# Optimization experiments

Measured on AMD Instinct MI355X. Metric: run time of the kernel, lower is better.

## Reference

```python
import jax, jax.numpy as jnp
import numpy as np

N_NODES = 100000
N_EDGES = 3200000
IN_DIM = 512
OUT_DIM = 256


def setup_inputs() -> dict:
    key = jax.random.key(0)
    k1, k2, k3, k4, k5 = jax.random.split(key, 5)
    features = jax.random.normal(k1, (N_NODES, IN_DIM), dtype=jnp.float32)
    adj_rows = jax.random.randint(k2, (N_EDGES,), 0, N_NODES, dtype=jnp.int32)
    adj_cols = jax.random.randint(k3, (N_EDGES,), 0, N_NODES, dtype=jnp.int32)
    # normalized adjacency values (e.g., 1/sqrt(d_i d_j)); random positive here
    adj_vals = jax.random.uniform(k4, (N_EDGES,), dtype=jnp.float32) * (1.0 / 32.0)
    # xavier uniform for kernel
    limit = np.sqrt(6.0 / (IN_DIM + OUT_DIM)).astype(np.float32)
    kernel = jax.random.uniform(k5, (IN_DIM, OUT_DIM), dtype=jnp.float32, minval=-limit, maxval=limit)
    bias = jnp.zeros((OUT_DIM,), dtype=jnp.float32)
    skip_weight = jnp.ones((OUT_DIM,), dtype=jnp.float32)
    return {
        "features": features,
        "adj_rows": adj_rows,
        "adj_cols": adj_cols,
        "adj_vals": adj_vals,
        "kernel": kernel,
        "bias": bias,
        "skip_weight": skip_weight,
    }


def reference(features, adj_rows, adj_cols, adj_vals, kernel, bias, skip_weight):
    # dense feature transform: [N, in] @ [in, out] -> [N, out]
    xw = jnp.matmul(features, kernel)
    # SpMM: aggregate[i] = sum_e val[e] * xw[col[e]] over edges with row[e] == i
    msgs = adj_vals[:, None] * xw[adj_cols]            # [E, out] gather
    agg = jax.ops.segment_sum(msgs, adj_rows, num_segments=N_NODES)  # [N, out] scatter-add
    out = xw * skip_weight + agg + bias                # skip scale + bias epilogue
    return jax.nn.selu(out)
```

## Files before the change

### kernel.cpp

```cpp
#include <hip/hip_runtime.h>
#include <hip/hip_bf16.h>
#include <cstdint>
#include <cstddef>

#define IN_DIM 512
#define OUT_DIM 256
#define BROWS 256
#define NBUCK_MAX 512

typedef __bf16 bf16x8 __attribute__((ext_vector_type(8)));
typedef float f32x4 __attribute__((ext_vector_type(4)));

__device__ __forceinline__ unsigned short f2bf(float f) {
    __bf16 h = (__bf16)f;
    return __builtin_bit_cast(unsigned short, h);
}
__device__ __forceinline__ float bf2f(unsigned short u) {
    unsigned int x = ((unsigned int)u) << 16;
    return __builtin_bit_cast(float, x);
}
__device__ __forceinline__ float selu(float x) {
    const float kScale = 1.0507009873554805f;
    const float kAlpha = 1.6732632423543772f;
    return (x > 0.f) ? kScale * x : kScale * kAlpha * (expf(x) - 1.f);
}

__global__ void k_convW(const float* __restrict__ W, unsigned short* __restrict__ Wt) {
    int idx = blockIdx.x * 256 + threadIdx.x;
    int n = idx & (OUT_DIM - 1);
    int k = idx >> 8;
    if (k < IN_DIM) Wt[n * IN_DIM + k] = f2bf(W[k * OUT_DIM + n]);
}

__launch_bounds__(512, 2)
__global__ void k_gemm(const float* __restrict__ A, const unsigned short* __restrict__ Wt,
                       signed char* __restrict__ xq, float* __restrict__ scales, int M) {
    __shared__ unsigned short lA[128 * 32];
    __shared__ unsigned short lB[256 * 32];
    __shared__ float lrm[128];
    const int t = threadIdx.x;
    const int wave = t >> 6, lane = t & 63;
    const int wr = wave >> 2, wc = wave & 3;
    const int m0 = blockIdx.x * 128;
    const int mlo = lane & 15, kq = lane >> 4;

    if (t < 128) lrm[t] = 0.f;

    f32x4 acc[4][4] = {};

    for (int k0 = 0; k0 < IN_DIM; k0 += 32) {
        #pragma unroll
        for (int p = 0; p < 2; ++p) {
            int idx = p * 512 + t;
            int r = idx >> 3, c4 = idx & 7;
            int gr = m0 + r; if (gr >= M) gr = M - 1;
            const float4 v = *reinterpret_cast<const float4*>(&A[(size_t)gr * IN_DIM + k0 + c4 * 4]);
            ushort4 u;
            u.x = f2bf(v.x); u.y = f2bf(v.y); u.z = f2bf(v.z); u.w = f2bf(v.w);
            *reinterpret_cast<ushort4*>(&lA[r * 32 + c4 * 4]) = u;
        }
        #pragma unroll
        for (int p = 0; p < 2; ++p) {
            int idx = p * 512 + t;
            int n = idx >> 2, c8 = idx & 3;
            const uint4 v = *reinterpret_cast<const uint4*>(&Wt[(size_t)n * IN_DIM + k0 + c8 * 8]);
            *reinterpret_cast<uint4*>(&lB[n * 32 + c8 * 8]) = v;
        }
        __syncthreads();

        bf16x8 af[4], bfr[4];
        #pragma unroll
        for (int mt = 0; mt < 4; ++mt)
            af[mt] = *reinterpret_cast<const bf16x8*>(&lA[(wr * 64 + mt * 16 + mlo) * 32 + kq * 8]);
        #pragma unroll
        for (int nt = 0; nt < 4; ++nt)
            bfr[nt] = *reinterpret_cast<const bf16x8*>(&lB[(wc * 64 + nt * 16 + mlo) * 32 + kq * 8]);
        #pragma unroll
        for (int mt = 0; mt < 4; ++mt)
            #pragma unroll
            for (int nt = 0; nt < 4; ++nt)
                acc[mt][nt] = __builtin_amdgcn_mfma_f32_16x16x32_bf16(af[mt], bfr[nt], acc[mt][nt], 0, 0, 0);
        __syncthreads();
    }

    #pragma unroll
    for (int mt = 0; mt < 4; ++mt) {
        #pragma unroll
        for (int i = 0; i < 4; ++i) {
            float m = fmaxf(fmaxf(fabsf(acc[mt][0][i]), fabsf(acc[mt][1][i])),
                            fmaxf(fabsf(acc[mt][2][i]), fabsf(acc[mt][3][i])));
            m = fmaxf(m, __shfl_xor(m, 1));
            m = fmaxf(m, __shfl_xor(m, 2));
            m = fmaxf(m, __shfl_xor(m, 4));
            m = fmaxf(m, __shfl_xor(m, 8));
            if (mlo == 0)
                atomicMax(reinterpret_cast<int*>(&lrm[wr * 64 + mt * 16 + kq * 4 + i]),
                          __float_as_int(m));
        }
    }
    __syncthreads();

    #pragma unroll
    for (int mt = 0; mt < 4; ++mt) {
        #pragma unroll
        for (int i = 0; i < 4; ++i) {
            const int rl = wr * 64 + mt * 16 + kq * 4 + i;
            const int row = m0 + rl;
            const float rm = lrm[rl];
            const float inv = (rm > 0.f) ? (127.f / rm) : 0.f;
            if (row < M) {
                #pragma unroll
                for (int nt = 0; nt < 4; ++nt) {
                    int q = (int)rintf(acc[mt][nt][i] * inv);
                    xq[(size_t)row * OUT_DIM + wc * 64 + nt * 16 + mlo] = (signed char)q;
                }
            }
        }
    }
    if (t < 128) {
        int row = m0 + t;
        if (row < M) scales[row] = lrm[t] * (1.f / 127.f);
    }
}

__launch_bounds__(512)
__global__ void k_bhist(const int* __restrict__ rows, int* __restrict__ bcnt, int E) {
    __shared__ int cnt[NBUCK_MAX];
    const int t = threadIdx.x;
    const int base = blockIdx.x * 8192;
    cnt[t] = 0;
    __syncthreads();
    #pragma unroll
    for (int p = 0; p < 4; ++p) {
        const int i = base + p * 2048 + (t << 2);
        if (i + 4 <= E) {
            int4 r4 = *reinterpret_cast<const int4*>(&rows[i]);
            atomicAdd(&cnt[r4.x >> 8], 1);
            atomicAdd(&cnt[r4.y >> 8], 1);
            atomicAdd(&cnt[r4.z >> 8], 1);
            atomicAdd(&cnt[r4.w >> 8], 1);
        } else if (i < E) {
            for (int j = i; j < E && j < i + 4; ++j) atomicAdd(&cnt[rows[j] >> 8], 1);
        }
    }
    __syncthreads();
    if (cnt[t] > 0) atomicAdd(&bcnt[t], cnt[t]);
}

__launch_bounds__(NBUCK_MAX)
__global__ void k_bscan(const int* __restrict__ bcnt, int* __restrict__ bbase,
                        int* __restrict__ bcursor, int nbuck, int E) {
    const int t = threadIdx.x;
    __shared__ int sh[NBUCK_MAX];
    int v = (t < nbuck) ? bcnt[t] : 0;
    sh[t] = v;
    __syncthreads();
    for (int off = 1; off < NBUCK_MAX; off <<= 1) {
        int x = (t >= off) ? sh[t - off] : 0;
        __syncthreads();
        sh[t] += x;
        __syncthreads();
    }
    int ex = sh[t] - v;
    bbase[t] = ex;
    bcursor[t] = ex;
    if (t == 0) bbase[NBUCK_MAX] = E;
}

__launch_bounds__(512)
__global__ void k_bin(const int* __restrict__ rows, const int* __restrict__ cols,
                      const float* __restrict__ vals, int* __restrict__ bcursor,
                      int2* __restrict__ binned, int E) {
    __shared__ int cnt[NBUCK_MAX];
    __shared__ int scn[NBUCK_MAX];
    __shared__ int dlt[NBUCK_MAX];
    const int t = threadIdx.x;
    const int base = blockIdx.x * 8192;

    cnt[t] = 0;
    __syncthreads();

    int er[16], ec[16];
    float ev[16];
    #pragma unroll
    for (int p = 0; p < 4; ++p) {
        const int i = base + p * 2048 + (t << 2);
        if (i + 4 <= E) {
            int4 r4 = *reinterpret_cast<const int4*>(&rows[i]);
            int4 c4 = *reinterpret_cast<const int4*>(&cols[i]);
            float4 v4 = *reinterpret_cast<const float4*>(&vals[i]);
            er[4*p+0] = r4.x; ec[4*p+0] = c4.x; ev[4*p+0] = v4.x;
            er[4*p+1] = r4.y; ec[4*p+1] = c4.y; ev[4*p+1] = v4.y;
            er[4*p+2] = r4.z; ec[4*p+2] = c4.z; ev[4*p+2] = v4.z;
            er[4*p+3] = r4.w; ec[4*p+3] = c4.w; ev[4*p+3] = v4.w;
        } else {
            #pragma unroll
            for (int j = 0; j < 4; ++j) {
                int idx = i + j;
                bool ok = idx < E;
                er[4*p+j] = ok ? rows[idx] : -1;
                ec[4*p+j] = ok ? cols[idx] : 0;
                ev[4*p+j] = ok ? vals[idx] : 0.f;
            }
        }
    }

    #pragma unroll
    for (int k = 0; k < 16; ++k)
        if (er[k] >= 0) atomicAdd(&cnt[er[k] >> 8], 1);
    __syncthreads();

    int v = cnt[t];
    scn[t] = v;
    __syncthreads();
    for (int off = 1; off < NBUCK_MAX; off <<= 1) {
        int x = (t >= off) ? scn[t - off] : 0;
        __syncthreads();
        scn[t] += x;
        __syncthreads();
    }
    int ex = scn[t] - v;

    int d = 0;
    if (v > 0) d = atomicAdd(&bcursor[t], v) - ex;
    dlt[t] = d;
    cnt[t] = ex;
    __syncthreads();

    #pragma unroll
    for (int k = 0; k < 16; ++k) {
        if (er[k] >= 0) {
            int b = er[k] >> 8;
            int lp = atomicAdd(&cnt[b], 1);
            binned[(size_t)(dlt[b] + lp)] =
                make_int2(ec[k] | ((er[k] & 255) << 17), __float_as_int(ev[k]));
        }
    }
}

__launch_bounds__(256)
__global__ void k_fine2(const int2* __restrict__ binned, const int* __restrict__ bbase,
                        const float* __restrict__ scales, int2* __restrict__ ecv,
                        int* __restrict__ rs, int M, int E, int nbuck) {
    __shared__ int lcnt[BROWS];
    __shared__ int lcur[BROWS];
    const int b = blockIdx.x, t = threadIdx.x;
    const int r0 = b * BROWS;
    lcnt[t] = 0;
    const int start = __builtin_amdgcn_readfirstlane(bbase[b]);
    const int end   = __builtin_amdgcn_readfirstlane(bbase[b + 1]);
    __syncthreads();

    for (int i = start + t; i < end; i += 256)
        atomicAdd(&lcnt[binned[i].x >> 17], 1);
    __syncthreads();

    int v = lcnt[t];
    lcur[t] = v;
    __syncthreads();
    for (int off = 1; off < 256; off <<= 1) {
        int x = (t >= off) ? lcur[t - off] : 0;
        __syncthreads();
        lcur[t] += x;
        __syncthreads();
    }
    int rowoff = start + (lcur[t] - v);
    if (r0 + t < M) rs[r0 + t] = rowoff;
    if (b == nbuck - 1 && t == 0) rs[M] = E;
    lcur[t] = rowoff;
    __syncthreads();

    for (int i = start + t; i < end; i += 256) {
        int2 rec = binned[i];
        int r = rec.x >> 17;
        int col = rec.x & 0x1FFFF;
        int pos = atomicAdd(&lcur[r], 1);
        ecv[pos] = make_int2(col, __float_as_int(__int_as_float(rec.y) * scales[col]));
    }
}

__global__ void k_hist(const int* __restrict__ rows, int* __restrict__ counts, int E) {
    int i = (blockIdx.x * 256 + threadIdx.x) * 4;
    if (i + 4 <= E) {
        int4 r = *reinterpret_cast<const int4*>(&rows[i]);
        atomicAdd(&counts[r.x], 1);
        atomicAdd(&counts[r.y], 1);
        atomicAdd(&counts[r.z], 1);
        atomicAdd(&counts[r.w], 1);
    } else {
        for (int j = i; j < E; ++j) atomicAdd(&counts[rows[j]], 1);
    }
}

__global__ void k_scan1(const int* __restrict__ counts, int* __restrict__ rs,
                        int* __restrict__ bsum, int N) {
    int b = blockIdx.x, t = threadIdx.x;
    int base = b * 1024 + t * 4;
    int4 v = make_int4(0, 0, 0, 0);
    if (base + 4 <= N) v = *reinterpret_cast<const int4*>(&counts[base]);
    else {
        if (base + 0 < N) v.x = counts[base + 0];
        if (base + 1 < N) v.y = counts[base + 1];
        if (base + 2 < N) v.z = counts[base + 2];
        if (base + 3 < N) v.w = counts[base + 3];
    }
    int s0 = v.x, s1 = s0 + v.y, s2 = s1 + v.z, s3 = s2 + v.w;
    __shared__ int sh[256];
    sh[t] = s3; __syncthreads();
    for (int off = 1; off < 256; off <<= 1) {
        int x = (t >= off) ? sh[t - off] : 0;
        __syncthreads();
        sh[t] += x;
        __syncthreads();
    }
    int ex = sh[t] - s3;
    if (base + 0 < N) rs[base + 0] = ex;
    if (base + 1 < N) rs[base + 1] = ex + s0;
    if (base + 2 < N) rs[base + 2] = ex + s1;
    if (base + 3 < N) rs[base + 3] = ex + s2;
    if (t == 255) bsum[b] = sh[255];
}

__global__ void k_scan2(const int* __restrict__ bsum, int* __restrict__ boff, int nb) {
    int t = threadIdx.x;
    __shared__ int sh[256];
    int v = (t < nb) ? bsum[t] : 0;
    sh[t] = v; __syncthreads();
    for (int off = 1; off < 256; off <<= 1) {
        int x = (t >= off) ? sh[t - off] : 0;
        __syncthreads();
        sh[t] += x;
        __syncthreads();
    }
    if (t < nb) boff[t] = sh[t] - v;
}

__global__ void k_scan3(int* __restrict__ rs, int* __restrict__ cursor,
                        const int* __restrict__ boff, int N, int E) {
    int b = blockIdx.x, t = threadIdx.x;
    int base = b * 1024 + t * 4;
    int o = boff[b];
    #pragma unroll
    for (int j = 0; j < 4; ++j) {
        if (base + j < N) {
            int v = rs[base + j] + o;
            rs[base + j] = v;
            cursor[base + j] = v;
        }
    }
    if (b == 0 && t == 0) rs[N] = E;
}

__global__ void k_scatter(const int* __restrict__ rows, const int* __restrict__ cols,
                          const float* __restrict__ vals, const float* __restrict__ scales,
                          int* __restrict__ cursor, int2* __restrict__ ecv, int E) {
    int i = (blockIdx.x * 256 + threadIdx.x) * 4;
    if (i + 4 <= E) {
        int4 r = *reinterpret_cast<const int4*>(&rows[i]);
        int4 c = *reinterpret_cast<const int4*>(&cols[i]);
        float4 v = *reinterpret_cast<const float4*>(&vals[i]);
        int p0 = atomicAdd(&cursor[r.x], 1); ecv[p0] = make_int2(c.x, __float_as_int(v.x * scales[c.x]));
        int p1 = atomicAdd(&cursor[r.y], 1); ecv[p1] = make_int2(c.y, __float_as_int(v.y * scales[c.y]));
        int p2 = atomicAdd(&cursor[r.z], 1); ecv[p2] = make_int2(c.z, __float_as_int(v.z * scales[c.z]));
        int p3 = atomicAdd(&cursor[r.w], 1); ecv[p3] = make_int2(c.w, __float_as_int(v.w * scales[c.w]));
    } else {
        for (int j = i; j < E; ++j) {
            int p = atomicAdd(&cursor[rows[j]], 1);
            ecv[p] = make_int2(cols[j], __float_as_int(vals[j] * scales[cols[j]]));
        }
    }
}

__launch_bounds__(256)
__global__ void k_agg(const signed char* __restrict__ xq,
                      const float* __restrict__ scales,
                      const int2* __restrict__ ecv,
                      const int* __restrict__ rs,
                      const float* __restrict__ skipw,
                      const float* __restrict__ bias,
                      float* __restrict__ out, int M) {
    const int wave = threadIdx.x >> 6, lane = threadIdx.x & 63;
    const int node = blockIdx.x * 4 + wave;
    if (node >= M) return;
    const int s = __builtin_amdgcn_readfirstlane(rs[node]);
    const int e = __builtin_amdgcn_readfirstlane(rs[node + 1]);
    const int d4 = lane * 4;

    float a0 = 0.f, a1 = 0.f, a2 = 0.f, a3 = 0.f;
    int p = s;
    constexpr int U = 8;
    for (; p + U <= e; p += U) {
        int   cs[U];
        float vs[U];
        #pragma unroll
        for (int u = 0; u < U; ++u) {
            int2 c = ecv[p + u];
            cs[u] = c.x; vs[u] = __int_as_float(c.y);
        }
        int g[U];
        #pragma unroll
        for (int u = 0; u < U; ++u)
            g[u] = *reinterpret_cast<const int*>(&xq[(size_t)cs[u] * OUT_DIM + d4]);
        #pragma unroll
        for (int u = 0; u < U; ++u) {
            a0 += vs[u] * (float)(signed char)(g[u]);
            a1 += vs[u] * (float)(signed char)(g[u] >> 8);
            a2 += vs[u] * (float)(signed char)(g[u] >> 16);
            a3 += vs[u] * (float)(g[u] >> 24);
        }
    }
    for (; p < e; ++p) {
        int2 c = ecv[p];
        float v = __int_as_float(c.y);
        int g = *reinterpret_cast<const int*>(&xq[(size_t)c.x * OUT_DIM + d4]);
        a0 += v * (float)(signed char)(g);
        a1 += v * (float)(signed char)(g >> 8);
        a2 += v * (float)(signed char)(g >> 16);
        a3 += v * (float)(g >> 24);
    }

    int w = *reinterpret_cast<const int*>(&xq[(size_t)node * OUT_DIM + d4]);
    float sc = scales[node];
    float x0 = (float)(signed char)(w)        * sc;
    float x1 = (float)(signed char)(w >> 8)   * sc;
    float x2 = (float)(signed char)(w >> 16)  * sc;
    float x3 = (float)(w >> 24)               * sc;

    float4 sw = *reinterpret_cast<const float4*>(&skipw[d4]);
    float4 bi = *reinterpret_cast<const float4*>(&bias[d4]);
    float4 r;
    r.x = selu(a0 + x0 * sw.x + bi.x);
    r.y = selu(a1 + x1 * sw.y + bi.y);
    r.z = selu(a2 + x2 * sw.z + bi.z);
    r.w = selu(a3 + x3 * sw.w + bi.w);
    *reinterpret_cast<float4*>(&out[(size_t)node * OUT_DIM + d4]) = r;
}

extern "C" void kernel_launch(void* const* d_in, const int* in_sizes, int n_in,
                              void* d_out, int out_size, void* d_ws, size_t ws_size,
                              hipStream_t stream) {
    const float* features = (const float*)d_in[0];
    const int*   adj_rows = (const int*)d_in[1];
    const int*   adj_cols = (const int*)d_in[2];
    const float* adj_vals = (const float*)d_in[3];
    const float* Wk       = (const float*)d_in[4];
    const float* bias     = (const float*)d_in[5];
    const float* skipw    = (const float*)d_in[6];
    float* out = (float*)d_out;

    const int M = in_sizes[0] / IN_DIM;
    const int E = in_sizes[1];

    char* w = (char*)d_ws;
    size_t off = 0;
    auto carve = [&](size_t bytes) -> void* {
        void* p = w + off;
        off = (off + bytes + 255) & ~(size_t)255;
        return p;
    };
    signed char* xq = (signed char*)carve((size_t)M * OUT_DIM);
    float* scales   = (float*)carve((size_t)M * 4);
    unsigned short* Wt = (unsigned short*)carve((size_t)IN_DIM * OUT_DIM * 2);
    int*  counts = (int*)carve((size_t)M * 4);
    int*  rs     = (int*)carve((size_t)(M + 1) * 4);
    int*  cursor = (int*)carve((size_t)M * 4);
    int*  bsum   = (int*)carve(256 * 4);
    int*  boff   = (int*)carve(256 * 4);
    int*  bcnt   = (int*)carve((NBUCK_MAX + 1) * 4);
    int*  bbase  = (int*)carve((NBUCK_MAX + 1) * 4);
    int*  bcur   = (int*)carve((NBUCK_MAX + 1) * 4);
    int2* ecv    = (int2*)carve((size_t)E * 8);
    int2* binned = (int2*)carve((size_t)E * 8);
    const int nbuck = (M + BROWS - 1) / BROWS;
    const bool use_binned = (off <= ws_size) && (nbuck <= NBUCK_MAX) && (M <= (1 << 17));

    k_convW<<<(IN_DIM * OUT_DIM + 255) / 256, 256, 0, stream>>>(Wk, Wt);
    k_gemm<<<(M + 127) / 128, 512, 0, stream>>>(features, Wt, xq, scales, M);

    if (use_binned) {
        hipMemsetAsync(bcnt, 0, (NBUCK_MAX + 1) * 4, stream);
        k_bhist<<<(E + 8191) / 8192, 512, 0, stream>>>(adj_rows, bcnt, E);
        k_bscan<<<1, NBUCK_MAX, 0, stream>>>(bcnt, bbase, bcur, nbuck, E);
        k_bin<<<(E + 8191) / 8192, 512, 0, stream>>>(adj_rows, adj_cols, adj_vals, bcur, binned, E);
        k_fine2<<<nbuck, 256, 0, stream>>>(binned, bbase, scales, ecv, rs, M, E, nbuck);
    } else {
        hipMemsetAsync(counts, 0, (size_t)M * 4, stream);
        k_hist<<<(E / 4 + 255) / 256, 256, 0, stream>>>(adj_rows, counts, E);
        int nb = (M + 1023) / 1024;
        k_scan1<<<nb, 256, 0, stream>>>(counts, rs, bsum, M);
        k_scan2<<<1, 256, 0, stream>>>(bsum, boff, nb);
        k_scan3<<<nb, 256, 0, stream>>>(rs, cursor, boff, M, E);
        k_scatter<<<(E / 4 + 255) / 256, 256, 0, stream>>>(adj_rows, adj_cols, adj_vals, scales, cursor, ecv, E);
    }

    k_agg<<<(M + 3) / 4, 256, 0, stream>>>(xq, scales, ecv, rs, skipw, bias, out, M);
}
```

Baseline: 567.0 us.

## Fuse fine binning into aggregation kernel using shared-memory per-bucket CSR

Replaces the k_fine2 pass, which wrote a global CSR edge array, with a k_aggb kernel. Each 512-thread block loads its 256-row bucket of binned edges, sorts them by row in LDS, and then aggregates and applies the SELU epilogue directly. The per-column scale multiply moves into k_bin, which removes one full read/write pass over the E edge records and one kernel launch. In exchange, each block processes 256 rows with only 8 waves, which gives far fewer blocks (about 391) and less parallelism for the gather-heavy aggregation. The large LDS footprint lowers occupancy, and there is a slow fallback path for overfull buckets.

```diff
diff --git a/kernel.cpp b/kernel.cpp
--- a/kernel.cpp
+++ b/kernel.cpp
@@ -7,6 +7,7 @@
 #define OUT_DIM 256
 #define BROWS 256
 #define NBUCK_MAX 512
+#define CAP 9216
 
 typedef __bf16 bf16x8 __attribute__((ext_vector_type(8)));
 typedef float f32x4 __attribute__((ext_vector_type(4)));
@@ -169,8 +170,8 @@
 
 __launch_bounds__(512)
 __global__ void k_bin(const int* __restrict__ rows, const int* __restrict__ cols,
-                      const float* __restrict__ vals, int* __restrict__ bcursor,
-                      int2* __restrict__ binned, int E) {
+                      const float* __restrict__ vals, const float* __restrict__ scales,
+                      int* __restrict__ bcursor, int2* __restrict__ binned, int E) {
     __shared__ int cnt[NBUCK_MAX];
     __shared__ int scn[NBUCK_MAX];
     __shared__ int dlt[NBUCK_MAX];
@@ -189,10 +190,10 @@
             int4 r4 = *reinterpret_cast<const int4*>(&rows[i]);
             int4 c4 = *reinterpret_cast<const int4*>(&cols[i]);
             float4 v4 = *reinterpret_cast<const float4*>(&vals[i]);
-            er[4*p+0] = r4.x; ec[4*p+0] = c4.x; ev[4*p+0] = v4.x;
-            er[4*p+1] = r4.y; ec[4*p+1] = c4.y; ev[4*p+1] = v4.y;
-            er[4*p+2] = r4.z; ec[4*p+2] = c4.z; ev[4*p+2] = v4.z;
-            er[4*p+3] = r4.w; ec[4*p+3] = c4.w; ev[4*p+3] = v4.w;
+            er[4*p+0] = r4.x; ec[4*p+0] = c4.x; ev[4*p+0] = v4.x * scales[c4.x];
+            er[4*p+1] = r4.y; ec[4*p+1] = c4.y; ev[4*p+1] = v4.y * scales[c4.y];
+            er[4*p+2] = r4.z; ec[4*p+2] = c4.z; ev[4*p+2] = v4.z * scales[c4.z];
+            er[4*p+3] = r4.w; ec[4*p+3] = c4.w; ev[4*p+3] = v4.w * scales[c4.w];
         } else {
             #pragma unroll
             for (int j = 0; j < 4; ++j) {
@@ -200,7 +201,7 @@
                 bool ok = idx < E;
                 er[4*p+j] = ok ? rows[idx] : -1;
                 ec[4*p+j] = ok ? cols[idx] : 0;
-                ev[4*p+j] = ok ? vals[idx] : 0.f;
+                ev[4*p+j] = ok ? vals[idx] * scales[cols[idx]] : 0.f;
             }
         }
     }
@@ -238,44 +239,132 @@
     }
 }
 
-__launch_bounds__(256)
-__global__ void k_fine2(const int2* __restrict__ binned, const int* __restrict__ bbase,
-                        const float* __restrict__ scales, int2* __restrict__ ecv,
-                        int* __restrict__ rs, int M, int E, int nbuck) {
-    __shared__ int lcnt[BROWS];
+__launch_bounds__(512)
+__global__ void k_aggb(const signed char* __restrict__ xq,
+                       const float* __restrict__ scales,
+                       const int2* __restrict__ binned,
+                       const int* __restrict__ bbase,
+                       const float* __restrict__ skipw,
+                       const float* __restrict__ bias,
+                       float* __restrict__ out, int M) {
+    __shared__ int2 lrec[CAP];
+    __shared__ int lrs[BROWS + 1];
     __shared__ int lcur[BROWS];
     const int b = blockIdx.x, t = threadIdx.x;
-    const int r0 = b * BROWS;
-    lcnt[t] = 0;
-    const int start = __builtin_amdgcn_readfirstlane(bbase[b]);
-    const int end   = __builtin_amdgcn_readfirstlane(bbase[b + 1]);
-    __syncthreads();
-
-    for (int i = start + t; i < end; i += 256)
-        atomicAdd(&lcnt[binned[i].x >> 17], 1);
-    __syncthreads();
-
-    int v = lcnt[t];
-    lcur[t] = v;
-    __syncthreads();
-    for (int off = 1; off < 256; off <<= 1) {
-        int x = (t >= off) ? lcur[t - off] : 0;
-        __syncthreads();
-        lcur[t] += x;
-        __syncthreads();
-    }
-    int rowoff = start + (lcur[t] - v);
-    if (r0 + t < M) rs[r0 + t] = rowoff;
-    if (b == nbuck - 1 && t == 0) rs[M] = E;
-    lcur[t] = rowoff;
-    __syncthreads();
-
-    for (int i = start + t; i < end; i += 256) {
-        int2 rec = binned[i];
-        int r = rec.x >> 17;
-        int col = rec.x & 0x1FFFF;
-        int pos = atomicAdd(&lcur[r], 1);
-        ecv[pos] = make_int2(col, __float_as_int(__int_as_float(rec.y) * scales[col]));
+    const int wave = t >> 6, lane = t & 63;
+    const int start = bbase[b], end = bbase[b + 1];
+    const int cnt = end - start;
+    const int d4 = lane * 4;
+
+    if (cnt <= CAP) {
+        if (t < BROWS) lcur[t] = 0;
+        __syncthreads();
+        for (int i = start + t; i < end; i += 512)
+            atomicAdd(&lcur[binned[i].x >> 17], 1);
+        __syncthreads();
+        int v = 0;
+        if (t < BROWS) { v = lcur[t]; lrs[t] = v; }
+        __syncthreads();
+        for (int off = 1; off < BROWS; off <<= 1) {
+            int x = 0;
+            if (t < BROWS && t >= off) x = lrs[t - off];
+            __syncthreads();
+            if (t < BROWS) lrs[t] += x;
+            __syncthreads();
+        }
+        int ex = 0;
+        if (t < BROWS) ex = lrs[t] - v;
+        __syncthreads();
+        if (t < BROWS) { lrs[t] = ex; lcur[t] = ex; }
+        if (t == 0) lrs[BROWS] = cnt;
+        __syncthreads();
+        for (int i = start + t; i < end; i += 512) {
+            int2 rec = binned[i];
+            int pos = atomicAdd(&lcur[rec.x >> 17], 1);
+            lrec[pos] = rec;
+        }
+        __syncthreads();
+        for (int rr = 0; rr < BROWS / 8; ++rr) {
+            const int r = wave * (BROWS / 8) + rr;
+            const int grow = b * BROWS + r;
+            if (grow >= M) continue;
+            const int s = lrs[r], e = lrs[r + 1];
+            float a0 = 0.f, a1 = 0.f, a2 = 0.f, a3 = 0.f;
+            int p = s;
+            for (; p + 8 <= e; p += 8) {
+                int cs[8]; float vs[8];
+                #pragma unroll
+                for (int u = 0; u < 8; ++u) {
+                    int2 c = lrec[p + u];
+                    cs[u] = c.x & 0x1FFFF; vs[u] = __int_as_float(c.y);
+                }
+                int g[8];
+                #pragma unroll
+                for (int u = 0; u < 8; ++u)
+                    g[u] = *reinterpret_cast<const int*>(&xq[(size_t)cs[u] * OUT_DIM + d4]);
+                #pragma unroll
+                for (int u = 0; u < 8; ++u) {
+                    a0 += vs[u] * (float)(signed char)(g[u]);
+                    a1 += vs[u] * (float)(signed char)(g[u] >> 8);
+                    a2 += vs[u] * (float)(signed char)(g[u] >> 16);
+                    a3 += vs[u] * (float)(g[u] >> 24);
+                }
+            }
+            for (; p < e; ++p) {
+                int2 c = lrec[p];
+                float v2 = __int_as_float(c.y);
+                int g = *reinterpret_cast<const int*>(&xq[(size_t)(c.x & 0x1FFFF) * OUT_DIM + d4]);
+                a0 += v2 * (float)(signed char)(g);
+                a1 += v2 * (float)(signed char)(g >> 8);
+                a2 += v2 * (float)(signed char)(g >> 16);
+                a3 += v2 * (float)(g >> 24);
+            }
+            int w = *reinterpret_cast<const int*>(&xq[(size_t)grow * OUT_DIM + d4]);
+            float sc = scales[grow];
+            float x0 = (float)(signed char)(w)        * sc;
+            float x1 = (float)(signed char)(w >> 8)   * sc;
+            float x2 = (float)(signed char)(w >> 16)  * sc;
+            float x3 = (float)(w >> 24)               * sc;
+            float4 sw = *reinterpret_cast<const float4*>(&skipw[d4]);
+            float4 bi = *reinterpret_cast<const float4*>(&bias[d4]);
+            float4 r4;
+            r4.x = selu(a0 + x0 * sw.x + bi.x);
+            r4.y = selu(a1 + x1 * sw.y + bi.y);
+            r4.z = selu(a2 + x2 * sw.z + bi.z);
+            r4.w = selu(a3 + x3 * sw.w + bi.w);
+            *reinterpret_cast<float4*>(&out[(size_t)grow * OUT_DIM + d4]) = r4;
+        }
+    } else {
+        for (int rr = 0; rr < BROWS / 8; ++rr) {
+            const int r = wave * (BROWS / 8) + rr;
+            const int grow = b * BROWS + r;
+            if (grow >= M) continue;
+            float a0 = 0.f, a1 = 0.f, a2 = 0.f, a3 = 0.f;
+            for (int i = start; i < end; ++i) {
+                int2 c = binned[i];
+                if ((c.x >> 17) != r) continue;
+                float v2 = __int_as_float(c.y);
+                int g = *reinterpret_cast<const int*>(&xq[(size_t)(c.x & 0x1FFFF) * OUT_DIM + d4]);
+                a0 += v2 * (float)(signed char)(g);
+                a1 += v2 * (float)(signed char)(g >> 8);
+                a2 += v2 * (float)(signed char)(g >> 16);
+                a3 += v2 * (float)(g >> 24);
+            }
+            int w = *reinterpret_cast<const int*>(&xq[(size_t)grow * OUT_DIM + d4]);
+            float sc = scales[grow];
+            float x0 = (float)(signed char)(w)        * sc;
+            float x1 = (float)(signed char)(w >> 8)   * sc;
+            float x2 = (float)(signed char)(w >> 16)  * sc;
+            float x3 = (float)(w >> 24)               * sc;
+            float4 sw = *reinterpret_cast<const float4*>(&skipw[d4]);
+            float4 bi = *reinterpret_cast<const float4*>(&bias[d4]);
+            float4 r4;
+            r4.x = selu(a0 + x0 * sw.x + bi.x);
+            r4.y = selu(a1 + x1 * sw.y + bi.y);
+            r4.z = selu(a2 + x2 * sw.z + bi.z);
+            r4.w = selu(a3 + x3 * sw.w + bi.w);
+            *reinterpret_cast<float4*>(&out[(size_t)grow * OUT_DIM + d4]) = r4;
+        }
     }
 }
 
@@ -481,8 +570,8 @@
         hipMemsetAsync(bcnt, 0, (NBUCK_MAX + 1) * 4, stream);
         k_bhist<<<(E + 8191) / 8192, 512, 0, stream>>>(adj_rows, bcnt, E);
         k_bscan<<<1, NBUCK_MAX, 0, stream>>>(bcnt, bbase, bcur, nbuck, E);
-        k_bin<<<(E + 8191) / 8192, 512, 0, stream>>>(adj_rows, adj_cols, adj_vals, bcur, binned, E);
-        k_fine2<<<nbuck, 256, 0, stream>>>(binned, bbase, scales, ecv, rs, M, E, nbuck);
+        k_bin<<<(E + 8191) / 8192, 512, 0, stream>>>(adj_rows, adj_cols, adj_vals, scales, bcur, binned, E);
+        k_aggb<<<nbuck, 512, 0, stream>>>(xq, scales, binned, bbase, skipw, bias, out, M);
     } else {
         hipMemsetAsync(counts, 0, (size_t)M * 4, stream);
         k_hist<<<(E / 4 + 255) / 256, 256, 0, stream>>>(adj_rows, counts, E);
@@ -491,7 +580,6 @@
         k_scan2<<<1, 256, 0, stream>>>(bsum, boff, nb);
         k_scan3<<<nb, 256, 0, stream>>>(rs, cursor, boff, M, E);
         k_scatter<<<(E / 4 + 255) / 256, 256, 0, stream>>>(adj_rows, adj_cols, adj_vals, scales, cursor, ecv, E);
-    }
-
-    k_agg<<<(M + 3) / 4, 256, 0, stream>>>(xq, scales, ecv, rs, skipw, bias, out, M);
-}
+        k_agg<<<(M + 3) / 4, 256, 0, stream>>>(xq, scales, ecv, rs, skipw, bias, out, M);
+    }
+}
```

New measurement: 578.2 us. No clear change (+2.0%).
